# Performance work log

Measured on AMD Instinct MI355X. Metric: run time of the kernel, lower is better.

The kernel has to match this reference:

```python
import jax, jax.numpy as jnp
import numpy as np
from jax import lax

NUM_ITER = 10
SMOOTH = 1.0


def _minpool(x, wh, ww):
    # stride-1 min pool with SAME padding (pad value +inf, ignored by min)
    return lax.reduce_window(x, np.inf, lax.min, (1, 1, wh, ww), (1, 1, 1, 1), 'SAME')


def _maxpool(x, wh, ww):
    return lax.reduce_window(x, -np.inf, lax.max, (1, 1, wh, ww), (1, 1, 1, 1), 'SAME')


def soft_erode(img):
    # min of separable 3x1 and 1x3 min-pools (== -maxpool(-img) in torch)
    return jnp.minimum(_minpool(img, 3, 1), _minpool(img, 1, 3))


def soft_dilate(img):
    return _maxpool(img, 3, 3)


def soft_open(img):
    return soft_dilate(soft_erode(img))


def soft_skeleton(img, num_iter=NUM_ITER):
    skel = jax.nn.relu(img - soft_open(img))
    x = img
    for _ in range(num_iter):  # fixed small unroll
        x = soft_erode(x)
        delta = jax.nn.relu(x - soft_open(x))
        skel = skel + jax.nn.relu(delta - skel * delta)
    return skel


def setup_inputs() -> dict:
    key = jax.random.key(0)
    k1, k2 = jax.random.split(key)
    pred = jax.random.normal(k1, (32, 1, 512, 512), dtype=jnp.float32)
    target = jax.random.uniform(k2, (32, 1, 512, 512), dtype=jnp.float32)
    return {"pred": pred, "target": target}


def reference(pred, target):
    pred_prob = jax.nn.sigmoid(pred)
    target = target.astype(pred_prob.dtype)
    skel_pred = soft_skeleton(pred_prob, NUM_ITER)
    skel_target = soft_skeleton(target, NUM_ITER)
    tprec = ((skel_pred * target).sum() + SMOOTH) / (skel_pred.sum() + SMOOTH)
    tsens = ((skel_target * pred_prob).sum() + SMOOTH) / (skel_target.sum() + SMOOTH)
    cl_dice = 2 * tprec * tsens / (tprec + tsens + 1e-07)
    return 1.0 - cl_dice
```

## Files before the change

kernel.cpp:

```cpp
#include <hip/hip_runtime.h>

#define H 512
#define W 512
#define TILE 64
#define NT 256
#define SW 104
#define SROWS 90
#define TPD (W / TILE)
#define NBANKS 16
#define BANK_STRIDE 16

typedef _Float16 h8 __attribute__((ext_vector_type(8)));
typedef _Float16 h4 __attribute__((ext_vector_type(4)));

__device__ __forceinline__ float sigmf(float x) {
  return 1.0f / (1.0f + __expf(-x));
}
__device__ __forceinline__ float4 ld4(const float* p) { return *(const float4*)p; }

__device__ __forceinline__ h8 min3v(h8 a, h8 b, h8 c) {
  return __builtin_elementwise_min(__builtin_elementwise_min(a, b), c);
}
__device__ __forceinline__ h8 max3v(h8 a, h8 b, h8 c) {
  return __builtin_elementwise_max(__builtin_elementwise_max(a, b), c);
}
__device__ __forceinline__ h8 shl1(h8 v, _Float16 e) {
  h8 r = __builtin_shufflevector(v, v, 7, 0, 1, 2, 3, 4, 5, 6);
  r[0] = e;
  return r;
}
__device__ __forceinline__ h8 shr1(h8 v, _Float16 e) {
  h8 r = __builtin_shufflevector(v, v, 1, 2, 3, 4, 5, 6, 7, 0);
  r[7] = e;
  return r;
}
__device__ __forceinline__ _Float16 hi_half(const _Float16* p) {
  unsigned v = *(const unsigned*)p;
  unsigned short s = (unsigned short)(v >> 16);
  return __builtin_bit_cast(_Float16, s);
}
__device__ __forceinline__ _Float16 lo_half(const _Float16* p) {
  unsigned v = *(const unsigned*)p;
  return __builtin_bit_cast(_Float16, (unsigned short)v);
}
__device__ __forceinline__ _Float16 hmax3(_Float16 a, _Float16 b, _Float16 c) {
  _Float16 m = a > b ? a : b;
  return m > c ? m : c;
}

__global__ __launch_bounds__(NT) void cl_skel_kernel(
    const float* __restrict__ pred, const float* __restrict__ target,
    double* __restrict__ sums) {
  __shared__ _Float16 buf0[SROWS * SW];
  __shared__ _Float16 buf1[SROWS * SW];
  __shared__ float rbuf[2][NT / 64];

  const int tid = threadIdx.x;
  const int tileIdx = blockIdx.x;
  const int batch = blockIdx.y;
  const bool isPred = (blockIdx.z == 0);
  const int tr = (tileIdx / TPD) * TILE;
  const int tc = (tileIdx % TPD) * TILE;
  const float* __restrict__ img = isPred ? pred : target;
  const float* __restrict__ other = isPred ? target : pred;
  const size_t base = (size_t)batch * (H * W);

  const bool border = (tr == 0) | (tc == 0) | (tr == H - TILE) | (tc == W - TILE);

  if (!border) {
    for (int it = tid; it < SROWS * 24; it += NT) {
      int row = it / 24, g = it - row * 24;
      int gr = tr - 13 + row;
      int gc = tc - 16 + 4 * g;
      float4 v = ld4(&img[base + (size_t)gr * W + gc]);
      if (isPred) {
        v.x = sigmf(v.x); v.y = sigmf(v.y); v.z = sigmf(v.z); v.w = sigmf(v.w);
      }
      h4 hv;
      hv[0] = (_Float16)v.x; hv[1] = (_Float16)v.y;
      hv[2] = (_Float16)v.z; hv[3] = (_Float16)v.w;
      *(h4*)(buf0 + row * SW + 4 * g) = hv;
    }
  } else {
    for (int it = tid; it < SROWS * 24; it += NT) {
      int row = it / 24, g = it - row * 24;
      int gr = min(max(tr - 13 + row, 0), H - 1);
      int gc = tc - 16 + 4 * g;
      float4 v;
      v.x = img[base + (size_t)gr * W + min(max(gc + 0, 0), W - 1)];
      v.y = img[base + (size_t)gr * W + min(max(gc + 1, 0), W - 1)];
      v.z = img[base + (size_t)gr * W + min(max(gc + 2, 0), W - 1)];
      v.w = img[base + (size_t)gr * W + min(max(gc + 3, 0), W - 1)];
      if (isPred) {
        v.x = sigmf(v.x); v.y = sigmf(v.y); v.z = sigmf(v.z); v.w = sigmf(v.w);
      }
      h4 hv;
      hv[0] = (_Float16)v.x; hv[1] = (_Float16)v.y;
      hv[2] = (_Float16)v.z; hv[3] = (_Float16)v.w;
      *(h4*)(buf0 + row * SW + 4 * g) = hv;
    }
  }
  __syncthreads();

  const int ty = tid >> 2;
  const int tg = tid & 3;
  const int rr = 13 + ty;
  const int c0 = 16 + 16 * tg;

  h8 skelE = (h8)(_Float16)0.0f;
  h8 skelF = (h8)(_Float16)0.0f;
  _Float16* src = buf0;
  _Float16* dst = buf1;

#pragma unroll 1
  for (int R = 11; R >= 1; --R) {
    const _Float16* ps = src + rr * SW + c0;
    h8 t0E = *(const h8*)ps;
    h8 t0F = *(const h8*)(ps + 8);

    const int rb = 13 - R;
    const int items = (32 + R) * 12;
    for (int it = tid; it < items; it += NT) {
      int rp = it / 12;
      int g = it - rp * 12;
      int r0 = rb + 2 * rp;
      const _Float16* s0 = src + (r0 - 1) * SW + 8 * g;
      h8 a = *(const h8*)(s0);
      h8 b = *(const h8*)(s0 + SW);
      h8 c = *(const h8*)(s0 + 2 * SW);
      h8 d = *(const h8*)(s0 + 3 * SW);
      _Float16 le0 = hi_half(s0 + SW - 2);
      _Float16 le1 = hi_half(s0 + 2 * SW - 2);
      _Float16 re0 = lo_half(s0 + SW + 8);
      _Float16 re1 = lo_half(s0 + 2 * SW + 8);
      h8 o0 = __builtin_elementwise_min(
          min3v(a, b, c),
          __builtin_elementwise_min(shl1(b, le0), shr1(b, re0)));
      h8 o1 = __builtin_elementwise_min(
          min3v(b, c, d),
          __builtin_elementwise_min(shl1(c, le1), shr1(c, re1)));
      *(h8*)(dst + r0 * SW + 8 * g) = o0;
      *(h8*)(dst + (r0 + 1) * SW + 8 * g) = o1;
    }
    __syncthreads();

    {
      const _Float16* pm = dst + (rr - 1) * SW + c0;
      h8 aE = *(const h8*)(pm),          aF = *(const h8*)(pm + 8);
      h8 bE = *(const h8*)(pm + SW),     bF = *(const h8*)(pm + SW + 8);
      h8 cE = *(const h8*)(pm + 2 * SW), cF = *(const h8*)(pm + 2 * SW + 8);
      _Float16 vl = hmax3(hi_half(pm - 2), hi_half(pm + SW - 2),
                          hi_half(pm + 2 * SW - 2));
      _Float16 vr = hmax3(lo_half(pm + 16), lo_half(pm + SW + 16),
                          lo_half(pm + 2 * SW + 16));
      h8 vmE = max3v(aE, bE, cE);
      h8 vmF = max3v(aF, bF, cF);
      h8 hE = max3v(shl1(vmE, vl), vmE, shr1(vmE, vmF[0]));
      h8 hF = max3v(shl1(vmF, vmE[7]), vmF, shr1(vmF, vr));
      h8 z = (h8)(_Float16)0.0f;
      h8 dE = __builtin_elementwise_max(t0E - hE, z);
      h8 dF = __builtin_elementwise_max(t0F - hF, z);
      skelE += __builtin_elementwise_max(dE - skelE * dE, z);
      skelF += __builtin_elementwise_max(dF - skelF * dF, z);
    }
    _Float16* t = src; src = dst; dst = t;
  }

  const float* orow = other + base + (size_t)(tr + ty) * W + tc + 16 * tg;
  float s0 = 0.0f, s1 = 0.0f;
#pragma unroll
  for (int q = 0; q < 4; ++q) {
    float4 o = ld4(orow + 4 * q);
    if (!isPred) {
      o.x = sigmf(o.x); o.y = sigmf(o.y); o.z = sigmf(o.z); o.w = sigmf(o.w);
    }
    float sk0, sk1, sk2, sk3;
    if (q < 2) {
      sk0 = (float)skelE[4 * q + 0]; sk1 = (float)skelE[4 * q + 1];
      sk2 = (float)skelE[4 * q + 2]; sk3 = (float)skelE[4 * q + 3];
    } else {
      sk0 = (float)skelF[4 * q - 8]; sk1 = (float)skelF[4 * q - 7];
      sk2 = (float)skelF[4 * q - 6]; sk3 = (float)skelF[4 * q - 5];
    }
    s0 += (sk0 + sk1) + (sk2 + sk3);
    s1 += (sk0 * o.x + sk1 * o.y) + (sk2 * o.z + sk3 * o.w);
  }

#pragma unroll
  for (int off = 32; off > 0; off >>= 1) {
    s0 += __shfl_down(s0, off, 64);
    s1 += __shfl_down(s1, off, 64);
  }
  const int wave = tid >> 6;
  const int lane = tid & 63;
  if (lane == 0) {
    rbuf[0][wave] = s0;
    rbuf[1][wave] = s1;
  }
  __syncthreads();
  if (tid == 0) {
    float t0 = 0.0f, t1 = 0.0f;
#pragma unroll
    for (int w = 0; w < NT / 64; ++w) {
      t0 += rbuf[0][w];
      t1 += rbuf[1][w];
    }
    const int bank = (int)(blockIdx.x & (NBANKS - 1));
    const int o2 = (isPred ? 0 : 2);
    atomicAdd(&sums[bank * BANK_STRIDE + o2], (double)t0);
    atomicAdd(&sums[bank * BANK_STRIDE + o2 + 1], (double)t1);
  }
}

__global__ void cl_finalize_kernel(const double* __restrict__ sums,
                                   float* __restrict__ out) {
  double s[4] = {0.0, 0.0, 0.0, 0.0};
  for (int b = 0; b < NBANKS; ++b)
    for (int j = 0; j < 4; ++j) s[j] += sums[b * BANK_STRIDE + j];
  double tprec = (s[1] + 1.0) / (s[0] + 1.0);
  double tsens = (s[3] + 1.0) / (s[2] + 1.0);
  double cl = 2.0 * tprec * tsens / (tprec + tsens + 1e-7);
  out[0] = (float)(1.0 - cl);
}

extern "C" void kernel_launch(void* const* d_in, const int* in_sizes, int n_in,
                              void* d_out, int out_size, void* d_ws,
                              size_t ws_size, hipStream_t stream) {
  const float* pred = (const float*)d_in[0];
  const float* target = (const float*)d_in[1];
  double* sums = (double*)d_ws;
  const int batch = in_sizes[0] / (H * W);

  hipMemsetAsync(d_ws, 0, NBANKS * BANK_STRIDE * sizeof(double), stream);
  dim3 grid(TPD * TPD, batch, 2);
  cl_skel_kernel<<<grid, NT, 0, stream>>>(pred, target, sums);
  cl_finalize_kernel<<<1, 1, 0, stream>>>(sums, (float*)d_out);
}
```

Baseline: 215.3 us.

## Double threads per tile, shrink erode region per pass, fuse finalize via last-block

Raises the block to 512 threads so each thread handles 8 columns instead of 16, and passes horizontal dilation neighbours between lanes with shuffles. Each erosion pass is templated on its radius and unrolled at compile time, so the processed column range shrinks as the needed halo shrinks, cutting shared-memory work. The separate finalize kernel is removed: a global counter picks the last block, which reduces the banked sums and writes the output. The trade-offs are more threads competing for shared memory and an extra atomic plus fences per block.

```diff
diff --git a/kernel.cpp b/kernel.cpp
--- a/kernel.cpp
+++ b/kernel.cpp
@@ -3,12 +3,10 @@
 #define H 512
 #define W 512
 #define TILE 64
-#define NT 256
+#define NT 512
 #define SW 104
 #define SROWS 90
 #define TPD (W / TILE)
-#define NBANKS 16
-#define BANK_STRIDE 16
 
 typedef _Float16 h8 __attribute__((ext_vector_type(8)));
 typedef _Float16 h4 __attribute__((ext_vector_type(4)));
@@ -36,8 +34,7 @@
 }
 __device__ __forceinline__ _Float16 hi_half(const _Float16* p) {
   unsigned v = *(const unsigned*)p;
-  unsigned short s = (unsigned short)(v >> 16);
-  return __builtin_bit_cast(_Float16, s);
+  return __builtin_bit_cast(_Float16, (unsigned short)(v >> 16));
 }
 __device__ __forceinline__ _Float16 lo_half(const _Float16* p) {
   unsigned v = *(const unsigned*)p;
@@ -47,13 +44,77 @@
   _Float16 m = a > b ? a : b;
   return m > c ? m : c;
 }
-
-__global__ __launch_bounds__(NT) void cl_skel_kernel(
+__device__ __forceinline__ unsigned dword_of(h8 v, int i) {
+  union { h8 h; unsigned u[4]; } cv;
+  cv.h = v;
+  return cv.u[i];
+}
+
+template <int R>
+__device__ __forceinline__ void erode_pass(const _Float16* __restrict__ src,
+                                           _Float16* __restrict__ dst, int tid) {
+  constexpr int rb = 13 - R;
+  constexpr int cs = (15 - R) & ~7;
+  constexpr int G = ((80 + R - cs) >> 3) + 1;
+  constexpr int ITEMS = (32 + R) * G;
+  for (int it = tid; it < ITEMS; it += NT) {
+    int rp = it / G;
+    int g = it - rp * G;
+    int r0 = rb + 2 * rp;
+    const _Float16* s0 = src + (r0 - 1) * SW + cs + 8 * g;
+    h8 a = *(const h8*)(s0);
+    h8 b = *(const h8*)(s0 + SW);
+    h8 c = *(const h8*)(s0 + 2 * SW);
+    h8 d = *(const h8*)(s0 + 3 * SW);
+    _Float16 le0 = hi_half(s0 + SW - 2);
+    _Float16 le1 = hi_half(s0 + 2 * SW - 2);
+    _Float16 re0 = lo_half(s0 + SW + 8);
+    _Float16 re1 = lo_half(s0 + 2 * SW + 8);
+    h8 o0 = __builtin_elementwise_min(
+        min3v(a, b, c),
+        __builtin_elementwise_min(shl1(b, le0), shr1(b, re0)));
+    h8 o1 = __builtin_elementwise_min(
+        min3v(b, c, d),
+        __builtin_elementwise_min(shl1(c, le1), shr1(c, re1)));
+    _Float16* d0 = dst + r0 * SW + cs + 8 * g;
+    *(h8*)(d0) = o0;
+    *(h8*)(d0 + SW) = o1;
+  }
+}
+
+__device__ __forceinline__ h8 dilate_update(const _Float16* __restrict__ dst,
+                                            int rr, int c0, int tg, h8 t0,
+                                            h8& skel) {
+  const _Float16* pm = dst + (rr - 1) * SW + c0;
+  h8 a = *(const h8*)(pm);
+  h8 b = *(const h8*)(pm + SW);
+  h8 c = *(const h8*)(pm + 2 * SW);
+  h8 vm = max3v(a, b, c);
+  unsigned nl = __shfl_up((int)dword_of(vm, 3), 1, 8);
+  unsigned nr = __shfl_down((int)dword_of(vm, 0), 1, 8);
+  _Float16 vl = __builtin_bit_cast(_Float16, (unsigned short)(nl >> 16));
+  _Float16 vr = __builtin_bit_cast(_Float16, (unsigned short)nr);
+  if (tg == 0) {
+    vl = hmax3(hi_half(pm - 2), hi_half(pm + SW - 2), hi_half(pm + 2 * SW - 2));
+  }
+  if (tg == 7) {
+    vr = hmax3(lo_half(pm + 8), lo_half(pm + SW + 8), lo_half(pm + 2 * SW + 8));
+  }
+  h8 h = max3v(shl1(vm, vl), vm, shr1(vm, vr));
+  h8 z = (h8)(_Float16)0.0f;
+  h8 d = __builtin_elementwise_max(t0 - h, z);
+  skel += __builtin_elementwise_max(d - skel * d, z);
+  return b;
+}
+
+__global__ __launch_bounds__(NT, 8) void cl_skel_kernel(
     const float* __restrict__ pred, const float* __restrict__ target,
-    double* __restrict__ sums) {
+    double* __restrict__ sums, unsigned* __restrict__ counter,
+    float* __restrict__ out) {
   __shared__ _Float16 buf0[SROWS * SW];
   __shared__ _Float16 buf1[SROWS * SW];
   __shared__ float rbuf[2][NT / 64];
+  __shared__ int lastFlag;
 
   const int tid = threadIdx.x;
   const int tileIdx = blockIdx.x;
@@ -102,86 +163,43 @@
   }
   __syncthreads();
 
-  const int ty = tid >> 2;
-  const int tg = tid & 3;
+  const int ty = tid >> 3;
+  const int tg = tid & 7;
   const int rr = 13 + ty;
-  const int c0 = 16 + 16 * tg;
-
-  h8 skelE = (h8)(_Float16)0.0f;
-  h8 skelF = (h8)(_Float16)0.0f;
-  _Float16* src = buf0;
-  _Float16* dst = buf1;
-
-#pragma unroll 1
-  for (int R = 11; R >= 1; --R) {
-    const _Float16* ps = src + rr * SW + c0;
-    h8 t0E = *(const h8*)ps;
-    h8 t0F = *(const h8*)(ps + 8);
-
-    const int rb = 13 - R;
-    const int items = (32 + R) * 12;
-    for (int it = tid; it < items; it += NT) {
-      int rp = it / 12;
-      int g = it - rp * 12;
-      int r0 = rb + 2 * rp;
-      const _Float16* s0 = src + (r0 - 1) * SW + 8 * g;
-      h8 a = *(const h8*)(s0);
-      h8 b = *(const h8*)(s0 + SW);
-      h8 c = *(const h8*)(s0 + 2 * SW);
-      h8 d = *(const h8*)(s0 + 3 * SW);
-      _Float16 le0 = hi_half(s0 + SW - 2);
-      _Float16 le1 = hi_half(s0 + 2 * SW - 2);
-      _Float16 re0 = lo_half(s0 + SW + 8);
-      _Float16 re1 = lo_half(s0 + 2 * SW + 8);
-      h8 o0 = __builtin_elementwise_min(
-          min3v(a, b, c),
-          __builtin_elementwise_min(shl1(b, le0), shr1(b, re0)));
-      h8 o1 = __builtin_elementwise_min(
-          min3v(b, c, d),
-          __builtin_elementwise_min(shl1(c, le1), shr1(c, re1)));
-      *(h8*)(dst + r0 * SW + 8 * g) = o0;
-      *(h8*)(dst + (r0 + 1) * SW + 8 * g) = o1;
-    }
-    __syncthreads();
-
-    {
-      const _Float16* pm = dst + (rr - 1) * SW + c0;
-      h8 aE = *(const h8*)(pm),          aF = *(const h8*)(pm + 8);
-      h8 bE = *(const h8*)(pm + SW),     bF = *(const h8*)(pm + SW + 8);
-      h8 cE = *(const h8*)(pm + 2 * SW), cF = *(const h8*)(pm + 2 * SW + 8);
-      _Float16 vl = hmax3(hi_half(pm - 2), hi_half(pm + SW - 2),
-                          hi_half(pm + 2 * SW - 2));
-      _Float16 vr = hmax3(lo_half(pm + 16), lo_half(pm + SW + 16),
-                          lo_half(pm + 2 * SW + 16));
-      h8 vmE = max3v(aE, bE, cE);
-      h8 vmF = max3v(aF, bF, cF);
-      h8 hE = max3v(shl1(vmE, vl), vmE, shr1(vmE, vmF[0]));
-      h8 hF = max3v(shl1(vmF, vmE[7]), vmF, shr1(vmF, vr));
-      h8 z = (h8)(_Float16)0.0f;
-      h8 dE = __builtin_elementwise_max(t0E - hE, z);
-      h8 dF = __builtin_elementwise_max(t0F - hF, z);
-      skelE += __builtin_elementwise_max(dE - skelE * dE, z);
-      skelF += __builtin_elementwise_max(dF - skelF * dF, z);
-    }
-    _Float16* t = src; src = dst; dst = t;
-  }
-
-  const float* orow = other + base + (size_t)(tr + ty) * W + tc + 16 * tg;
+  const int c0 = 16 + 8 * tg;
+
+  h8 skel = (h8)(_Float16)0.0f;
+  h8 t0 = *(const h8*)(buf0 + rr * SW + c0);
+
+#define STEP(R, S, D)                          \
+  {                                            \
+    erode_pass<R>(S, D, tid);                  \
+    __syncthreads();                           \
+    t0 = dilate_update(D, rr, c0, tg, t0, skel); \
+  }
+  STEP(11, buf0, buf1)
+  STEP(10, buf1, buf0)
+  STEP(9, buf0, buf1)
+  STEP(8, buf1, buf0)
+  STEP(7, buf0, buf1)
+  STEP(6, buf1, buf0)
+  STEP(5, buf0, buf1)
+  STEP(4, buf1, buf0)
+  STEP(3, buf0, buf1)
+  STEP(2, buf1, buf0)
+  STEP(1, buf0, buf1)
+#undef STEP
+
+  const float* orow = other + base + (size_t)(tr + ty) * W + tc + 8 * tg;
   float s0 = 0.0f, s1 = 0.0f;
 #pragma unroll
-  for (int q = 0; q < 4; ++q) {
+  for (int q = 0; q < 2; ++q) {
     float4 o = ld4(orow + 4 * q);
     if (!isPred) {
       o.x = sigmf(o.x); o.y = sigmf(o.y); o.z = sigmf(o.z); o.w = sigmf(o.w);
     }
-    float sk0, sk1, sk2, sk3;
-    if (q < 2) {
-      sk0 = (float)skelE[4 * q + 0]; sk1 = (float)skelE[4 * q + 1];
-      sk2 = (float)skelE[4 * q + 2]; sk3 = (float)skelE[4 * q + 3];
-    } else {
-      sk0 = (float)skelF[4 * q - 8]; sk1 = (float)skelF[4 * q - 7];
-      sk2 = (float)skelF[4 * q - 6]; sk3 = (float)skelF[4 * q - 5];
-    }
+    float sk0 = (float)skel[4 * q + 0], sk1 = (float)skel[4 * q + 1];
+    float sk2 = (float)skel[4 * q + 2], sk3 = (float)skel[4 * q + 3];
     s0 += (sk0 + sk1) + (sk2 + sk3);
     s1 += (sk0 * o.x + sk1 * o.y) + (sk2 * o.z + sk3 * o.w);
   }
@@ -192,35 +210,47 @@
     s1 += __shfl_down(s1, off, 64);
   }
   const int wave = tid >> 6;
-  const int lane = tid & 63;
-  if (lane == 0) {
+  if ((tid & 63) == 0) {
     rbuf[0][wave] = s0;
     rbuf[1][wave] = s1;
   }
   __syncthreads();
+
+  const unsigned nblocks = gridDim.x * gridDim.y * gridDim.z;
   if (tid == 0) {
-    float t0 = 0.0f, t1 = 0.0f;
+    float t0s = 0.0f, t1s = 0.0f;
 #pragma unroll
     for (int w = 0; w < NT / 64; ++w) {
-      t0 += rbuf[0][w];
-      t1 += rbuf[1][w];
-    }
-    const int bank = (int)(blockIdx.x & (NBANKS - 1));
+      t0s += rbuf[0][w];
+      t1s += rbuf[1][w];
+    }
+    const int bank = (int)(blockIdx.x & 15);
     const int o2 = (isPred ? 0 : 2);
-    atomicAdd(&sums[bank * BANK_STRIDE + o2], (double)t0);
-    atomicAdd(&sums[bank * BANK_STRIDE + o2 + 1], (double)t1);
-  }
-}
-
-__global__ void cl_finalize_kernel(const double* __restrict__ sums,
-                                   float* __restrict__ out) {
-  double s[4] = {0.0, 0.0, 0.0, 0.0};
-  for (int b = 0; b < NBANKS; ++b)
-    for (int j = 0; j < 4; ++j) s[j] += sums[b * BANK_STRIDE + j];
-  double tprec = (s[1] + 1.0) / (s[0] + 1.0);
-  double tsens = (s[3] + 1.0) / (s[2] + 1.0);
-  double cl = 2.0 * tprec * tsens / (tprec + tsens + 1e-7);
-  out[0] = (float)(1.0 - cl);
+    atomicAdd(&sums[bank * 16 + o2], (double)t0s);
+    atomicAdd(&sums[bank * 16 + o2 + 1], (double)t1s);
+    __threadfence();
+    unsigned old = atomicAdd(counter, 1u);
+    lastFlag = (old == nblocks - 1) ? 1 : 0;
+  }
+  __syncthreads();
+
+  if (lastFlag && tid < 64) {
+    __threadfence();
+    int b = tid >> 2, j = tid & 3;
+    double v = atomicAdd(&sums[b * 16 + j], 0.0);
+#pragma unroll
+    for (int off = 4; off < 64; off <<= 1) v += __shfl_down(v, off, 64);
+    double s0d = __shfl(v, 0, 64);
+    double s1d = __shfl(v, 1, 64);
+    double s2d = __shfl(v, 2, 64);
+    double s3d = __shfl(v, 3, 64);
+    if (tid == 0) {
+      double tprec = (s1d + 1.0) / (s0d + 1.0);
+      double tsens = (s3d + 1.0) / (s2d + 1.0);
+      double cl = 2.0 * tprec * tsens / (tprec + tsens + 1e-7);
+      out[0] = (float)(1.0 - cl);
+    }
+  }
 }
 
 extern "C" void kernel_launch(void* const* d_in, const int* in_sizes, int n_in,
@@ -229,10 +259,11 @@
   const float* pred = (const float*)d_in[0];
   const float* target = (const float*)d_in[1];
   double* sums = (double*)d_ws;
+  unsigned* counter = (unsigned*)((char*)d_ws + 2048);
   const int batch = in_sizes[0] / (H * W);
 
-  hipMemsetAsync(d_ws, 0, NBANKS * BANK_STRIDE * sizeof(double), stream);
+  hipMemsetAsync(d_ws, 0, 2048 + 64, stream);
   dim3 grid(TPD * TPD, batch, 2);
-  cl_skel_kernel<<<grid, NT, 0, stream>>>(pred, target, sums);
-  cl_finalize_kernel<<<1, 1, 0, stream>>>(sums, (float*)d_out);
-}
+  cl_skel_kernel<<<grid, NT, 0, stream>>>(pred, target, sums, counter,
+                                          (float*)d_out);
+}
```

Result: slower. 827.8 us (+284.6%).

## Fuse finalize into main kernel, shrink erode columns, reuse eroded center rows

Applied to the files above, without the earlier changes.

Three changes. The separate finalize launch is removed: each block bumps a global counter after its atomic adds, and the last block to arrive reduces the banked sums and writes the loss. The erosion pass now skips the outer column groups once the halo radius is small (R<8), which trims shared-memory work in later iterations. The t0 values are taken from the middle row already loaded for the dilation instead of being reloaded from shared memory each iteration. In exchange, every block pays a threadfence and an extra counter atomic.

```diff
diff --git a/kernel.cpp b/kernel.cpp
--- a/kernel.cpp
+++ b/kernel.cpp
@@ -7,8 +7,6 @@
 #define SW 104
 #define SROWS 90
 #define TPD (W / TILE)
-#define NBANKS 16
-#define BANK_STRIDE 16
 
 typedef _Float16 h8 __attribute__((ext_vector_type(8)));
 typedef _Float16 h4 __attribute__((ext_vector_type(4)));
@@ -36,8 +34,7 @@
 }
 __device__ __forceinline__ _Float16 hi_half(const _Float16* p) {
   unsigned v = *(const unsigned*)p;
-  unsigned short s = (unsigned short)(v >> 16);
-  return __builtin_bit_cast(_Float16, s);
+  return __builtin_bit_cast(_Float16, (unsigned short)(v >> 16));
 }
 __device__ __forceinline__ _Float16 lo_half(const _Float16* p) {
   unsigned v = *(const unsigned*)p;
@@ -48,12 +45,45 @@
   return m > c ? m : c;
 }
 
+template <int CS, int G>
+__device__ __forceinline__ void erode_g(const _Float16* __restrict__ src,
+                                        _Float16* __restrict__ dst, int R,
+                                        int tid) {
+  const int rb = 13 - R;
+  const int items = (32 + R) * G;
+  for (int it = tid; it < items; it += NT) {
+    int rp = it / G;
+    int g = it - rp * G;
+    int r0 = rb + 2 * rp;
+    const _Float16* s0 = src + (r0 - 1) * SW + CS + 8 * g;
+    h8 a = *(const h8*)(s0);
+    h8 b = *(const h8*)(s0 + SW);
+    h8 c = *(const h8*)(s0 + 2 * SW);
+    h8 d = *(const h8*)(s0 + 3 * SW);
+    _Float16 le0 = hi_half(s0 + SW - 2);
+    _Float16 le1 = hi_half(s0 + 2 * SW - 2);
+    _Float16 re0 = lo_half(s0 + SW + 8);
+    _Float16 re1 = lo_half(s0 + 2 * SW + 8);
+    h8 o0 = __builtin_elementwise_min(
+        min3v(a, b, c),
+        __builtin_elementwise_min(shl1(b, le0), shr1(b, re0)));
+    h8 o1 = __builtin_elementwise_min(
+        min3v(b, c, d),
+        __builtin_elementwise_min(shl1(c, le1), shr1(c, re1)));
+    _Float16* d0 = dst + r0 * SW + CS + 8 * g;
+    *(h8*)(d0) = o0;
+    *(h8*)(d0 + SW) = o1;
+  }
+}
+
 __global__ __launch_bounds__(NT) void cl_skel_kernel(
     const float* __restrict__ pred, const float* __restrict__ target,
-    double* __restrict__ sums) {
+    double* __restrict__ sums, unsigned* __restrict__ counter,
+    float* __restrict__ out) {
   __shared__ _Float16 buf0[SROWS * SW];
   __shared__ _Float16 buf1[SROWS * SW];
   __shared__ float rbuf[2][NT / 64];
+  __shared__ int lastFlag;
 
   const int tid = threadIdx.x;
   const int tileIdx = blockIdx.x;
@@ -109,39 +139,16 @@
 
   h8 skelE = (h8)(_Float16)0.0f;
   h8 skelF = (h8)(_Float16)0.0f;
+  h8 t0E = *(const h8*)(buf0 + rr * SW + c0);
+  h8 t0F = *(const h8*)(buf0 + rr * SW + c0 + 8);
+
   _Float16* src = buf0;
   _Float16* dst = buf1;
 
 #pragma unroll 1
   for (int R = 11; R >= 1; --R) {
-    const _Float16* ps = src + rr * SW + c0;
-    h8 t0E = *(const h8*)ps;
-    h8 t0F = *(const h8*)(ps + 8);
-
-    const int rb = 13 - R;
-    const int items = (32 + R) * 12;
-    for (int it = tid; it < items; it += NT) {
-      int rp = it / 12;
-      int g = it - rp * 12;
-      int r0 = rb + 2 * rp;
-      const _Float16* s0 = src + (r0 - 1) * SW + 8 * g;
-      h8 a = *(const h8*)(s0);
-      h8 b = *(const h8*)(s0 + SW);
-      h8 c = *(const h8*)(s0 + 2 * SW);
-      h8 d = *(const h8*)(s0 + 3 * SW);
-      _Float16 le0 = hi_half(s0 + SW - 2);
-      _Float16 le1 = hi_half(s0 + 2 * SW - 2);
-      _Float16 re0 = lo_half(s0 + SW + 8);
-      _Float16 re1 = lo_half(s0 + 2 * SW + 8);
-      h8 o0 = __builtin_elementwise_min(
-          min3v(a, b, c),
-          __builtin_elementwise_min(shl1(b, le0), shr1(b, re0)));
-      h8 o1 = __builtin_elementwise_min(
-          min3v(b, c, d),
-          __builtin_elementwise_min(shl1(c, le1), shr1(c, re1)));
-      *(h8*)(dst + r0 * SW + 8 * g) = o0;
-      *(h8*)(dst + (r0 + 1) * SW + 8 * g) = o1;
-    }
+    if (R >= 8) erode_g<0, 12>(src, dst, R, tid);
+    else        erode_g<8, 10>(src, dst, R, tid);
     __syncthreads();
 
     {
@@ -162,6 +169,8 @@
       h8 dF = __builtin_elementwise_max(t0F - hF, z);
       skelE += __builtin_elementwise_max(dE - skelE * dE, z);
       skelF += __builtin_elementwise_max(dF - skelF * dF, z);
+      t0E = bE;
+      t0F = bF;
     }
     _Float16* t = src; src = dst; dst = t;
   }
@@ -192,35 +201,47 @@
     s1 += __shfl_down(s1, off, 64);
   }
   const int wave = tid >> 6;
-  const int lane = tid & 63;
-  if (lane == 0) {
+  if ((tid & 63) == 0) {
     rbuf[0][wave] = s0;
     rbuf[1][wave] = s1;
   }
   __syncthreads();
+
+  const unsigned nblocks = gridDim.x * gridDim.y * gridDim.z;
   if (tid == 0) {
-    float t0 = 0.0f, t1 = 0.0f;
+    float t0s = 0.0f, t1s = 0.0f;
 #pragma unroll
     for (int w = 0; w < NT / 64; ++w) {
-      t0 += rbuf[0][w];
-      t1 += rbuf[1][w];
-    }
-    const int bank = (int)(blockIdx.x & (NBANKS - 1));
+      t0s += rbuf[0][w];
+      t1s += rbuf[1][w];
+    }
+    const int bank = (int)(blockIdx.x & 15);
     const int o2 = (isPred ? 0 : 2);
-    atomicAdd(&sums[bank * BANK_STRIDE + o2], (double)t0);
-    atomicAdd(&sums[bank * BANK_STRIDE + o2 + 1], (double)t1);
-  }
-}
-
-__global__ void cl_finalize_kernel(const double* __restrict__ sums,
-                                   float* __restrict__ out) {
-  double s[4] = {0.0, 0.0, 0.0, 0.0};
-  for (int b = 0; b < NBANKS; ++b)
-    for (int j = 0; j < 4; ++j) s[j] += sums[b * BANK_STRIDE + j];
-  double tprec = (s[1] + 1.0) / (s[0] + 1.0);
-  double tsens = (s[3] + 1.0) / (s[2] + 1.0);
-  double cl = 2.0 * tprec * tsens / (tprec + tsens + 1e-7);
-  out[0] = (float)(1.0 - cl);
+    atomicAdd(&sums[bank * 16 + o2], (double)t0s);
+    atomicAdd(&sums[bank * 16 + o2 + 1], (double)t1s);
+    __threadfence();
+    unsigned old = atomicAdd(counter, 1u);
+    lastFlag = (old == nblocks - 1) ? 1 : 0;
+  }
+  __syncthreads();
+
+  if (lastFlag && tid < 64) {
+    __threadfence();
+    int b = tid >> 2, j = tid & 3;
+    double v = atomicAdd(&sums[b * 16 + j], 0.0);
+#pragma unroll
+    for (int off = 4; off < 64; off <<= 1) v += __shfl_down(v, off, 64);
+    double s0d = __shfl(v, 0, 64);
+    double s1d = __shfl(v, 1, 64);
+    double s2d = __shfl(v, 2, 64);
+    double s3d = __shfl(v, 3, 64);
+    if (tid == 0) {
+      double tprec = (s1d + 1.0) / (s0d + 1.0);
+      double tsens = (s3d + 1.0) / (s2d + 1.0);
+      double cl = 2.0 * tprec * tsens / (tprec + tsens + 1e-7);
+      out[0] = (float)(1.0 - cl);
+    }
+  }
 }
 
 extern "C" void kernel_launch(void* const* d_in, const int* in_sizes, int n_in,
@@ -229,10 +250,11 @@
   const float* pred = (const float*)d_in[0];
   const float* target = (const float*)d_in[1];
   double* sums = (double*)d_ws;
+  unsigned* counter = (unsigned*)((char*)d_ws + 2048);
   const int batch = in_sizes[0] / (H * W);
 
-  hipMemsetAsync(d_ws, 0, NBANKS * BANK_STRIDE * sizeof(double), stream);
+  hipMemsetAsync(d_ws, 0, 2048 + 64, stream);
   dim3 grid(TPD * TPD, batch, 2);
-  cl_skel_kernel<<<grid, NT, 0, stream>>>(pred, target, sums);
-  cl_finalize_kernel<<<1, 1, 0, stream>>>(sums, (float*)d_out);
-}
+  cl_skel_kernel<<<grid, NT, 0, stream>>>(pred, target, sums, counter,
+                                          (float*)d_out);
+}
```

Result: slower. 262.4 us (+21.9%).
